# Kernel optimization log

Measured on AMD Instinct MI355X. Metric: run time of the kernel, lower is better.

## Reference

```python
import jax, jax.numpy as jnp
import numpy as np

GRID = 512
F_FEAT = 32
CORE = 16
N_PTS = 2097152
SCALE = 0.1


def _bilinear_sample(plane, coords):
    """plane: (F, H, W); coords: (N, 2) with (x, y) in [-1, 1], align_corners=True.
    Returns (F, N)."""
    F_, H, W = plane.shape
    x = (coords[:, 0] + 1.0) * 0.5 * (W - 1)
    y = (coords[:, 1] + 1.0) * 0.5 * (H - 1)
    x0f = jnp.floor(x)
    y0f = jnp.floor(y)
    wx = x - x0f  # (N,)
    wy = y - y0f
    x0 = jnp.clip(x0f.astype(jnp.int32), 0, W - 1)
    x1 = jnp.clip(x0 + 1, 0, W - 1)
    y0 = jnp.clip(y0f.astype(jnp.int32), 0, H - 1)
    y1 = jnp.clip(y0 + 1, 0, H - 1)
    v00 = plane[:, y0, x0]  # (F, N)
    v01 = plane[:, y0, x1]
    v10 = plane[:, y1, x0]
    v11 = plane[:, y1, x1]
    return (v00 * (1.0 - wx) * (1.0 - wy)
            + v01 * wx * (1.0 - wy)
            + v10 * (1.0 - wx) * wy
            + v11 * wx * wy)


def setup_inputs() -> dict:
    key = jax.random.key(0)
    k1, k2, k3, k4, k5 = jax.random.split(key, 5)
    coords_plane = jax.random.uniform(
        k1, (3, 1, N_PTS, 1, 2), dtype=jnp.float32, minval=-1.0, maxval=1.0)
    plane_xy = SCALE * jax.random.normal(k2, (1, F_FEAT, GRID, GRID), dtype=jnp.float32)
    plane_yz = SCALE * jax.random.normal(k3, (1, F_FEAT, GRID, GRID), dtype=jnp.float32)
    plane_xz = SCALE * jax.random.normal(k4, (1, F_FEAT, GRID, GRID), dtype=jnp.float32)
    core_tensor = jax.random.normal(k5, (CORE, F_FEAT), dtype=jnp.float32)
    return {"coords_plane": coords_plane, "plane_xy": plane_xy,
            "plane_yz": plane_yz, "plane_xz": plane_xz,
            "core_tensor": core_tensor}


def reference(coords_plane, plane_xy, plane_yz, plane_xz, core_tensor):
    # coords_plane: (3, 1, N, 1, 2) -> (3, N, 2)
    c = coords_plane.reshape(3, -1, 2)
    f_xy = _bilinear_sample(plane_xy[0], c[0])  # (F, N)
    f_yz = _bilinear_sample(plane_yz[0], c[1])
    f_xz = _bilinear_sample(plane_xz[0], c[2])
    prod = f_xy * f_yz * f_xz                   # (F, N)
    # sum over core dim: out[f, n] = (sum_k core[k, f]) * prod[f, n]
    scale = jnp.sum(core_tensor, axis=0)        # (F,)
    out = (scale[:, None] * prod).T             # (N, F)
    return out
```

## Files before the change

kernel.cpp:

```cpp
#include <hip/hip_runtime.h>
#include <hip/hip_fp16.h>

#define N_PTS 2097152
#define GRID_ 512
#define F_FEAT 32
#define HW (GRID_ * GRID_)
#define HWF ((size_t)HW * F_FEAT)

#define NBINS 64
#define BIN_SHIFT 3
#define BIN_CAP 40960
#define CUR_STRIDE 32
#define PTS_PER_BLOCK 1024
#define SEGCAP 64
#define BPB 640

typedef float f32x4 __attribute__((ext_vector_type(4)));
typedef unsigned long long u64;

__global__ void td_scale_kernel(const float* __restrict__ core,
                                float* __restrict__ scale) {
    int f = threadIdx.x;
    float s = 0.0f;
#pragma unroll
    for (int k = 0; k < 16; ++k) s += core[k * F_FEAT + f];
    scale[f] = s;
}

__global__ void td_transpose_kernel(const float* __restrict__ pxy,
                                    const float* __restrict__ pyz,
                                    const float* __restrict__ pxz,
                                    const float* __restrict__ scale,
                                    __half* __restrict__ wsh) {
    __shared__ float tile[32][33];
    const int plane = blockIdx.z;
    const float* src = (plane == 0) ? pxy : ((plane == 1) ? pyz : pxz);
    __half* dst = wsh + (size_t)plane * HWF;
    const int y = blockIdx.y;
    const int x0 = blockIdx.x * 32;

    for (int i = threadIdx.y; i < 32; i += 8) {
        tile[i][threadIdx.x] =
            src[(size_t)i * HW + (size_t)y * GRID_ + x0 + threadIdx.x];
    }
    __syncthreads();
    const float sc = (plane == 0) ? scale[threadIdx.x] : 1.0f;
    for (int i = threadIdx.y; i < 32; i += 8) {
        dst[((size_t)(y * GRID_ + x0 + i)) * F_FEAT + threadIdx.x] =
            __float2half(tile[threadIdx.x][i] * sc);
    }
}

__global__ void td_zero_kernel(int* __restrict__ cursor) {
    for (int i = threadIdx.x; i < 3 * NBINS * CUR_STRIDE; i += 256) cursor[i] = 0;
}

__global__ __launch_bounds__(256) void td_bin_kernel(
    const float2* __restrict__ coords, int* __restrict__ cursor,
    u64* __restrict__ recs) {
    __shared__ int lhist[NBINS];
    __shared__ int lbase[NBINS];
    __shared__ u64 lseg[NBINS][SEGCAP];
    const int pl = blockIdx.y;
    const int tid = threadIdx.x;
    const int base_p = blockIdx.x * PTS_PER_BLOCK;
    if (tid < NBINS) lhist[tid] = 0;
    __syncthreads();

    u64 myrec[4];
    int mybin[4], myslot[4];
#pragma unroll
    for (int k = 0; k < 4; ++k) {
        const int p = base_p + k * 256 + tid;
        const float2 c = coords[(size_t)pl * N_PTS + p];
        const float xf = (c.x + 1.0f) * 0.5f * (float)(GRID_ - 1);
        const float yf = (c.y + 1.0f) * 0.5f * (float)(GRID_ - 1);
        const float x0f = floorf(xf);
        const float y0f = floorf(yf);
        const float wx = xf - x0f;
        const float wy = yf - y0f;
        int x0 = min(max((int)x0f, 0), GRID_ - 1);
        int y0 = min(max((int)y0f, 0), GRID_ - 1);
        const int qwx = min(4095, (int)(wx * 4096.0f + 0.5f));
        const int qwy = min(4095, (int)(wy * 4096.0f + 0.5f));
        const int bin = y0 >> BIN_SHIFT;
        myrec[k] = (u64)p | ((u64)x0 << 21) | ((u64)y0 << 30) |
                   ((u64)qwx << 39) | ((u64)qwy << 51);
        mybin[k] = bin;
        myslot[k] = atomicAdd(&lhist[bin], 1);
    }
    __syncthreads();

    if (tid < NBINS) {
        const int cnt = lhist[tid];
        lbase[tid] =
            (cnt > 0) ? atomicAdd(&cursor[(pl * NBINS + tid) * CUR_STRIDE], cnt)
                      : 0;
    }
#pragma unroll
    for (int k = 0; k < 4; ++k)
        if (myslot[k] < SEGCAP) lseg[mybin[k]][myslot[k]] = myrec[k];
    __syncthreads();

#pragma unroll
    for (int k = 0; k < 4; ++k) {
        if (myslot[k] >= SEGCAP) {
            const int gslot = lbase[mybin[k]] + myslot[k];
            if (gslot < BIN_CAP)
                recs[((size_t)pl * NBINS + mybin[k]) * BIN_CAP + gslot] =
                    myrec[k];
        }
    }
    for (int b = 0; b < NBINS; ++b) {
        const int cnt = min(lhist[b], SEGCAP);
        const int gb = lbase[b];
        for (int r = tid; r < cnt; r += 256) {
            if (gb + r < BIN_CAP)
                recs[((size_t)pl * NBINS + b) * BIN_CAP + gb + r] = lseg[b][r];
        }
    }
}

__device__ __forceinline__ void td_sample_core(u64 r, int fq,
                                               const f32x4* __restrict__ tp,
                                               float* s, int* pid_out) {
    const int pid = (int)(r & 0x1FFFFF);
    const int x0 = (int)((r >> 21) & 511);
    const int y0 = (int)((r >> 30) & 511);
    const float wx = (float)((int)((r >> 39) & 4095)) * (1.0f / 4096.0f);
    const float wy = (float)((int)((r >> 51) & 4095)) * (1.0f / 4096.0f);
    const int x1 = min(x0 + 1, GRID_ - 1);
    const int y1 = min(y0 + 1, GRID_ - 1);

    const f32x4 r00 = tp[(size_t)(y0 * GRID_ + x0) * 4 + fq];
    const f32x4 r01 = tp[(size_t)(y0 * GRID_ + x1) * 4 + fq];
    const f32x4 r10 = tp[(size_t)(y1 * GRID_ + x0) * 4 + fq];
    const f32x4 r11 = tp[(size_t)(y1 * GRID_ + x1) * 4 + fq];

    const float w00 = (1.0f - wx) * (1.0f - wy);
    const float w01 = wx * (1.0f - wy);
    const float w10 = (1.0f - wx) * wy;
    const float w11 = wx * wy;

    const half2* h00 = reinterpret_cast<const half2*>(&r00);
    const half2* h01 = reinterpret_cast<const half2*>(&r01);
    const half2* h10 = reinterpret_cast<const half2*>(&r10);
    const half2* h11 = reinterpret_cast<const half2*>(&r11);
#pragma unroll
    for (int j = 0; j < 4; ++j) {
        const float2 f00 = __half22float2(h00[j]);
        const float2 f01 = __half22float2(h01[j]);
        const float2 f10 = __half22float2(h10[j]);
        const float2 f11 = __half22float2(h11[j]);
        s[2 * j] = f00.x * w00 + f01.x * w01 + f10.x * w10 + f11.x * w11;
        s[2 * j + 1] = f00.y * w00 + f01.y * w01 + f10.y * w10 + f11.y * w11;
    }
    *pid_out = pid;
}

__device__ __forceinline__ int td_bin_of_block(int i, int* sub) {
    const int xcd = i & 7;
    const int j = i >> 3;
    const int g = j / BPB;
    *sub = j - g * BPB;
    return g * 8 + xcd;
}

__global__ __launch_bounds__(256) void td_sample_plane_kernel(
    const u64* __restrict__ recs, const int* __restrict__ cursor,
    const f32x4* __restrict__ ws4, f32x4* __restrict__ featline) {
    const int pl = blockIdx.y + 1;
    int sub;
    const int bin = td_bin_of_block(blockIdx.x, &sub);
    const int slot = sub * 64 + (threadIdx.x >> 2);
    const int fq = threadIdx.x & 3;
    const int cnt = min(cursor[(pl * NBINS + bin) * CUR_STRIDE], BIN_CAP);
    if (slot >= cnt) return;

    const u64 r = recs[((size_t)pl * NBINS + bin) * BIN_CAP + slot];
    float s[8];
    int pid;
    td_sample_core(r, fq, ws4 + (size_t)pl * (HWF / 8), s, &pid);

    union {
        f32x4 v;
        half2 h[4];
    } u;
#pragma unroll
    for (int j = 0; j < 4; ++j) u.h[j] = __floats2half2_rn(s[2 * j], s[2 * j + 1]);
    __builtin_nontemporal_store(
        u.v, &featline[(size_t)pid * 8 + (pl - 1) * 4 + fq]);
}

__global__ __launch_bounds__(256) void td_sample_combine_kernel(
    const u64* __restrict__ recs, const int* __restrict__ cursor,
    const f32x4* __restrict__ ws4, const f32x4* __restrict__ featline,
    f32x4* __restrict__ out) {
    int sub;
    const int bin = td_bin_of_block(blockIdx.x, &sub);
    const int slot = sub * 64 + (threadIdx.x >> 2);
    const int fq = threadIdx.x & 3;
    const int cnt = min(cursor[bin * CUR_STRIDE], BIN_CAP);
    if (slot >= cnt) return;

    const u64 r = recs[(size_t)bin * BIN_CAP + slot];
    float s[8];
    int pid;
    td_sample_core(r, fq, ws4, s, &pid);

    union {
        f32x4 v;
        half2 h[4];
    } f1, f2;
    f1.v = featline[(size_t)pid * 8 + fq];
    f2.v = featline[(size_t)pid * 8 + 4 + fq];

    f32x4 o0, o1;
    float rr[8];
#pragma unroll
    for (int j = 0; j < 4; ++j) {
        const float2 a = __half22float2(f1.h[j]);
        const float2 b = __half22float2(f2.h[j]);
        rr[2 * j] = s[2 * j] * a.x * b.x;
        rr[2 * j + 1] = s[2 * j + 1] * a.y * b.y;
    }
    o0.x = rr[0]; o0.y = rr[1]; o0.z = rr[2]; o0.w = rr[3];
    o1.x = rr[4]; o1.y = rr[5]; o1.z = rr[6]; o1.w = rr[7];
    __builtin_nontemporal_store(o0, &out[(size_t)pid * 8 + fq * 2]);
    __builtin_nontemporal_store(o1, &out[(size_t)pid * 8 + fq * 2 + 1]);
}

__global__ __launch_bounds__(256) void td_sample_kernel(
    const float2* __restrict__ coords, const f32x4* __restrict__ ws4,
    f32x4* __restrict__ out) {
    const int tid = blockIdx.x * 256 + threadIdx.x;
    const int p = tid >> 2;
    const int fq = tid & 3;

    const float2 c0 = coords[p];
    const float2 c1 = coords[N_PTS + p];
    const float2 c2 = coords[2 * N_PTS + p];

    size_t idx[3][4];
    float w[3][4];
    const float2 cc[3] = {c0, c1, c2};
#pragma unroll
    for (int pl = 0; pl < 3; ++pl) {
        const float xf = (cc[pl].x + 1.0f) * 0.5f * (float)(GRID_ - 1);
        const float yf = (cc[pl].y + 1.0f) * 0.5f * (float)(GRID_ - 1);
        const float x0f = floorf(xf);
        const float y0f = floorf(yf);
        const float wx = xf - x0f;
        const float wy = yf - y0f;
        int x0 = min(max((int)x0f, 0), GRID_ - 1);
        int y0 = min(max((int)y0f, 0), GRID_ - 1);
        const int x1 = min(x0 + 1, GRID_ - 1);
        const int y1 = min(y0 + 1, GRID_ - 1);
        const size_t base = (size_t)pl * (HWF / 8);
        idx[pl][0] = base + (size_t)(y0 * GRID_ + x0) * 4 + fq;
        idx[pl][1] = base + (size_t)(y0 * GRID_ + x1) * 4 + fq;
        idx[pl][2] = base + (size_t)(y1 * GRID_ + x0) * 4 + fq;
        idx[pl][3] = base + (size_t)(y1 * GRID_ + x1) * 4 + fq;
        w[pl][0] = (1.0f - wx) * (1.0f - wy);
        w[pl][1] = wx * (1.0f - wy);
        w[pl][2] = (1.0f - wx) * wy;
        w[pl][3] = wx * wy;
    }

    f32x4 v[3][4];
#pragma unroll
    for (int pl = 0; pl < 3; ++pl)
#pragma unroll
        for (int cnr = 0; cnr < 4; ++cnr) v[pl][cnr] = ws4[idx[pl][cnr]];

    float prod[8];
#pragma unroll
    for (int j = 0; j < 8; ++j) prod[j] = 1.0f;
#pragma unroll
    for (int pl = 0; pl < 3; ++pl) {
        const half2* h0 = reinterpret_cast<const half2*>(&v[pl][0]);
        const half2* h1 = reinterpret_cast<const half2*>(&v[pl][1]);
        const half2* h2 = reinterpret_cast<const half2*>(&v[pl][2]);
        const half2* h3 = reinterpret_cast<const half2*>(&v[pl][3]);
#pragma unroll
        for (int j = 0; j < 4; ++j) {
            const float2 f00 = __half22float2(h0[j]);
            const float2 f01 = __half22float2(h1[j]);
            const float2 f10 = __half22float2(h2[j]);
            const float2 f11 = __half22float2(h3[j]);
            prod[2 * j] *= f00.x * w[pl][0] + f01.x * w[pl][1] +
                           f10.x * w[pl][2] + f11.x * w[pl][3];
            prod[2 * j + 1] *= f00.y * w[pl][0] + f01.y * w[pl][1] +
                               f10.y * w[pl][2] + f11.y * w[pl][3];
        }
    }

    f32x4 o0, o1;
    o0.x = prod[0]; o0.y = prod[1]; o0.z = prod[2]; o0.w = prod[3];
    o1.x = prod[4]; o1.y = prod[5]; o1.z = prod[6]; o1.w = prod[7];
    __builtin_nontemporal_store(o0, &out[(size_t)tid * 2]);
    __builtin_nontemporal_store(o1, &out[(size_t)tid * 2 + 1]);
}

__global__ __launch_bounds__(256) void td_fallback_kernel(
    const float* __restrict__ coords, const float* __restrict__ pxy,
    const float* __restrict__ pyz, const float* __restrict__ pxz,
    const float* __restrict__ core, float* __restrict__ out) {
    const int tid = blockIdx.x * 256 + threadIdx.x;
    const int p = tid >> 5;
    const int f = tid & 31;

    float s = 0.0f;
#pragma unroll
    for (int k = 0; k < 16; ++k) s += core[k * F_FEAT + f];

    float prod = s;
    const float* planes[3] = {pxy, pyz, pxz};
#pragma unroll
    for (int plane = 0; plane < 3; ++plane) {
        const float cx = coords[((size_t)plane * N_PTS + p) * 2 + 0];
        const float cy = coords[((size_t)plane * N_PTS + p) * 2 + 1];
        const float xf = (cx + 1.0f) * 0.5f * (float)(GRID_ - 1);
        const float yf = (cy + 1.0f) * 0.5f * (float)(GRID_ - 1);
        const float x0f = floorf(xf);
        const float y0f = floorf(yf);
        const float wx = xf - x0f;
        const float wy = yf - y0f;
        int x0 = min(max((int)x0f, 0), GRID_ - 1);
        int y0 = min(max((int)y0f, 0), GRID_ - 1);
        const int x1 = min(x0 + 1, GRID_ - 1);
        const int y1 = min(y0 + 1, GRID_ - 1);
        const float* src = planes[plane] + (size_t)f * HW;
        const float v00 = src[y0 * GRID_ + x0];
        const float v01 = src[y0 * GRID_ + x1];
        const float v10 = src[y1 * GRID_ + x0];
        const float v11 = src[y1 * GRID_ + x1];
        prod *= v00 * (1.0f - wx) * (1.0f - wy) + v01 * wx * (1.0f - wy) +
                v10 * (1.0f - wx) * wy + v11 * wx * wy;
    }
    out[(size_t)p * F_FEAT + f] = prod;
}

extern "C" void kernel_launch(void* const* d_in, const int* in_sizes, int n_in,
                              void* d_out, int out_size, void* d_ws,
                              size_t ws_size, hipStream_t stream) {
    const float* coords = (const float*)d_in[0];
    const float* pxy = (const float*)d_in[1];
    const float* pyz = (const float*)d_in[2];
    const float* pxz = (const float*)d_in[3];
    const float* core = (const float*)d_in[4];
    float* out = (float*)d_out;

    size_t off = 0;
    auto alloc = [&off](size_t bytes) {
        size_t o = off;
        off = (off + bytes + 255) & ~(size_t)255;
        return o;
    };
    const size_t off_wsh = alloc(3 * HWF * sizeof(__half));
    const size_t off_scale = alloc(32 * sizeof(float));
    const size_t need_r4 = off;
    const size_t off_cur = alloc((size_t)3 * NBINS * CUR_STRIDE * sizeof(int));
    const size_t off_recs = alloc((size_t)3 * NBINS * BIN_CAP * sizeof(u64));
    const size_t off_feat = alloc((size_t)N_PTS * 128);
    const size_t need_full = off;

    char* ws = (char*)d_ws;

    if (ws_size >= need_r4) {
        __half* wsh = (__half*)(ws + off_wsh);
        float* scale = (float*)(ws + off_scale);
        td_scale_kernel<<<1, 32, 0, stream>>>(core, scale);
        td_transpose_kernel<<<dim3(GRID_ / 32, GRID_, 3), dim3(32, 8), 0,
                              stream>>>(pxy, pyz, pxz, scale, wsh);
        if (ws_size >= need_full) {
            int* cursor = (int*)(ws + off_cur);
            u64* recs = (u64*)(ws + off_recs);
            f32x4* featline = (f32x4*)(ws + off_feat);
            td_zero_kernel<<<1, 256, 0, stream>>>(cursor);
            td_bin_kernel<<<dim3(N_PTS / PTS_PER_BLOCK, 3), 256, 0, stream>>>(
                (const float2*)coords, cursor, recs);
            td_sample_plane_kernel<<<dim3(NBINS * BPB, 2), 256, 0, stream>>>(
                recs, cursor, (const f32x4*)wsh, featline);
            td_sample_combine_kernel<<<NBINS * BPB, 256, 0, stream>>>(
                recs, cursor, (const f32x4*)wsh, (const f32x4*)featline,
                (f32x4*)out);
        } else {
            td_sample_kernel<<<N_PTS * 4 / 256, 256, 0, stream>>>(
                (const float2*)coords, (const f32x4*)wsh, (f32x4*)out);
        }
    } else {
        td_fallback_kernel<<<N_PTS * 32 / 256, 256, 0, stream>>>(
            coords, pxy, pyz, pxz, core, out);
    }
}
```

Before: 378.5 us.

## Index intermediate plane features by plane-0 sorted slot instead of point id

```diff
diff --git a/kernel.cpp b/kernel.cpp
--- a/kernel.cpp
+++ b/kernel.cpp
@@ -55,13 +55,12 @@
     for (int i = threadIdx.x; i < 3 * NBINS * CUR_STRIDE; i += 256) cursor[i] = 0;
 }
 
-__global__ __launch_bounds__(256) void td_bin_kernel(
+__global__ __launch_bounds__(256) void td_bin0_kernel(
     const float2* __restrict__ coords, int* __restrict__ cursor,
-    u64* __restrict__ recs) {
+    u64* __restrict__ recs0, int* __restrict__ s0map) {
     __shared__ int lhist[NBINS];
     __shared__ int lbase[NBINS];
     __shared__ u64 lseg[NBINS][SEGCAP];
-    const int pl = blockIdx.y;
     const int tid = threadIdx.x;
     const int base_p = blockIdx.x * PTS_PER_BLOCK;
     if (tid < NBINS) lhist[tid] = 0;
@@ -72,7 +71,7 @@
 #pragma unroll
     for (int k = 0; k < 4; ++k) {
         const int p = base_p + k * 256 + tid;
-        const float2 c = coords[(size_t)pl * N_PTS + p];
+        const float2 c = coords[p];
         const float xf = (c.x + 1.0f) * 0.5f * (float)(GRID_ - 1);
         const float yf = (c.y + 1.0f) * 0.5f * (float)(GRID_ - 1);
         const float x0f = floorf(xf);
@@ -94,8 +93,74 @@
     if (tid < NBINS) {
         const int cnt = lhist[tid];
         lbase[tid] =
-            (cnt > 0) ? atomicAdd(&cursor[(pl * NBINS + tid) * CUR_STRIDE], cnt)
-                      : 0;
+            (cnt > 0) ? atomicAdd(&cursor[tid * CUR_STRIDE], cnt) : 0;
+    }
+#pragma unroll
+    for (int k = 0; k < 4; ++k)
+        if (myslot[k] < SEGCAP) lseg[mybin[k]][myslot[k]] = myrec[k];
+    __syncthreads();
+
+#pragma unroll
+    for (int k = 0; k < 4; ++k) {
+        const int p = base_p + k * 256 + tid;
+        int gslot = lbase[mybin[k]] + myslot[k];
+        if (gslot >= BIN_CAP) gslot = BIN_CAP - 1;
+        const int s0 = mybin[k] * BIN_CAP + gslot;
+        s0map[p] = s0;
+        if (myslot[k] >= SEGCAP) recs0[s0] = myrec[k];
+    }
+    for (int b = 0; b < NBINS; ++b) {
+        const int cnt = min(lhist[b], SEGCAP);
+        const int gb = lbase[b];
+        for (int r = tid; r < cnt; r += 256) {
+            if (gb + r < BIN_CAP) recs0[(size_t)b * BIN_CAP + gb + r] = lseg[b][r];
+        }
+    }
+}
+
+__global__ __launch_bounds__(256) void td_bin12_kernel(
+    const float2* __restrict__ coords, const int* __restrict__ s0map,
+    int* __restrict__ cursor, u64* __restrict__ recs12) {
+    __shared__ int lhist[NBINS];
+    __shared__ int lbase[NBINS];
+    __shared__ u64 lseg[NBINS][SEGCAP];
+    const int pl = blockIdx.y + 1;
+    const int tid = threadIdx.x;
+    const int base_p = blockIdx.x * PTS_PER_BLOCK;
+    if (tid < NBINS) lhist[tid] = 0;
+    __syncthreads();
+
+    u64 myrec[4];
+    int mybin[4], myslot[4];
+#pragma unroll
+    for (int k = 0; k < 4; ++k) {
+        const int p = base_p + k * 256 + tid;
+        const float2 c = coords[(size_t)pl * N_PTS + p];
+        const int s0 = s0map[p];
+        const float xf = (c.x + 1.0f) * 0.5f * (float)(GRID_ - 1);
+        const float yf = (c.y + 1.0f) * 0.5f * (float)(GRID_ - 1);
+        const float x0f = floorf(xf);
+        const float y0f = floorf(yf);
+        const float wx = xf - x0f;
+        const float wy = yf - y0f;
+        int x0 = min(max((int)x0f, 0), GRID_ - 1);
+        int y0 = min(max((int)y0f, 0), GRID_ - 1);
+        const int qwx = min(4095, (int)(wx * 4096.0f + 0.5f));
+        const int qwy = min(4095, (int)(wy * 4096.0f + 0.5f));
+        const int bin = y0 >> BIN_SHIFT;
+        myrec[k] = (u64)s0 | ((u64)x0 << 22) | ((u64)y0 << 31) |
+                   ((u64)qwx << 40) | ((u64)qwy << 52);
+        mybin[k] = bin;
+        myslot[k] = atomicAdd(&lhist[bin], 1);
+    }
+    __syncthreads();
+
+    if (tid < NBINS) {
+        const int cnt = lhist[tid];
+        lbase[tid] =
+            (cnt > 0)
+                ? atomicAdd(&cursor[((pl * NBINS) + tid) * CUR_STRIDE], cnt)
+                : 0;
     }
 #pragma unroll
     for (int k = 0; k < 4; ++k)
@@ -107,7 +172,7 @@
         if (myslot[k] >= SEGCAP) {
             const int gslot = lbase[mybin[k]] + myslot[k];
             if (gslot < BIN_CAP)
-                recs[((size_t)pl * NBINS + mybin[k]) * BIN_CAP + gslot] =
+                recs12[(((size_t)(pl - 1) * NBINS + mybin[k]) * BIN_CAP) + gslot] =
                     myrec[k];
         }
     }
@@ -116,19 +181,16 @@
         const int gb = lbase[b];
         for (int r = tid; r < cnt; r += 256) {
             if (gb + r < BIN_CAP)
-                recs[((size_t)pl * NBINS + b) * BIN_CAP + gb + r] = lseg[b][r];
+                recs12[((size_t)(pl - 1) * NBINS + b) * BIN_CAP + gb + r] =
+                    lseg[b][r];
         }
     }
 }
 
-__device__ __forceinline__ void td_sample_core(u64 r, int fq,
+__device__ __forceinline__ void td_sample_core(int x0, int y0, float wx,
+                                               float wy, int fq,
                                                const f32x4* __restrict__ tp,
-                                               float* s, int* pid_out) {
-    const int pid = (int)(r & 0x1FFFFF);
-    const int x0 = (int)((r >> 21) & 511);
-    const int y0 = (int)((r >> 30) & 511);
-    const float wx = (float)((int)((r >> 39) & 4095)) * (1.0f / 4096.0f);
-    const float wy = (float)((int)((r >> 51) & 4095)) * (1.0f / 4096.0f);
+                                               float* s) {
     const int x1 = min(x0 + 1, GRID_ - 1);
     const int y1 = min(y0 + 1, GRID_ - 1);
 
@@ -155,7 +217,6 @@
         s[2 * j] = f00.x * w00 + f01.x * w01 + f10.x * w10 + f11.x * w11;
         s[2 * j + 1] = f00.y * w00 + f01.y * w01 + f10.y * w10 + f11.y * w11;
     }
-    *pid_out = pid;
 }
 
 __device__ __forceinline__ int td_bin_of_block(int i, int* sub) {
@@ -166,9 +227,9 @@
     return g * 8 + xcd;
 }
 
-__global__ __launch_bounds__(256) void td_sample_plane_kernel(
-    const u64* __restrict__ recs, const int* __restrict__ cursor,
-    const f32x4* __restrict__ ws4, f32x4* __restrict__ featline) {
+__global__ __launch_bounds__(256) void td_sample12_kernel(
+    const u64* __restrict__ recs12, const int* __restrict__ cursor,
+    const f32x4* __restrict__ ws4, f32x4* __restrict__ feat) {
     const int pl = blockIdx.y + 1;
     int sub;
     const int bin = td_bin_of_block(blockIdx.x, &sub);
@@ -177,10 +238,15 @@
     const int cnt = min(cursor[(pl * NBINS + bin) * CUR_STRIDE], BIN_CAP);
     if (slot >= cnt) return;
 
-    const u64 r = recs[((size_t)pl * NBINS + bin) * BIN_CAP + slot];
+    const u64 r = recs12[((size_t)(pl - 1) * NBINS + bin) * BIN_CAP + slot];
+    const int s0 = (int)(r & 0x3FFFFF);
+    const int x0 = (int)((r >> 22) & 511);
+    const int y0 = (int)((r >> 31) & 511);
+    const float wx = (float)((int)((r >> 40) & 4095)) * (1.0f / 4096.0f);
+    const float wy = (float)((int)((r >> 52) & 4095)) * (1.0f / 4096.0f);
+
     float s[8];
-    int pid;
-    td_sample_core(r, fq, ws4 + (size_t)pl * (HWF / 8), s, &pid);
+    td_sample_core(x0, y0, wx, wy, fq, ws4 + (size_t)pl * (HWF / 8), s);
 
     union {
         f32x4 v;
@@ -188,13 +254,12 @@
     } u;
 #pragma unroll
     for (int j = 0; j < 4; ++j) u.h[j] = __floats2half2_rn(s[2 * j], s[2 * j + 1]);
-    __builtin_nontemporal_store(
-        u.v, &featline[(size_t)pid * 8 + (pl - 1) * 4 + fq]);
-}
-
-__global__ __launch_bounds__(256) void td_sample_combine_kernel(
-    const u64* __restrict__ recs, const int* __restrict__ cursor,
-    const f32x4* __restrict__ ws4, const f32x4* __restrict__ featline,
+    __builtin_nontemporal_store(u.v, &feat[(size_t)s0 * 8 + (pl - 1) * 4 + fq]);
+}
+
+__global__ __launch_bounds__(256) void td_combine_kernel(
+    const u64* __restrict__ recs0, const int* __restrict__ cursor,
+    const f32x4* __restrict__ ws4, const f32x4* __restrict__ feat,
     f32x4* __restrict__ out) {
     int sub;
     const int bin = td_bin_of_block(blockIdx.x, &sub);
@@ -203,19 +268,24 @@
     const int cnt = min(cursor[bin * CUR_STRIDE], BIN_CAP);
     if (slot >= cnt) return;
 
-    const u64 r = recs[(size_t)bin * BIN_CAP + slot];
+    const size_t s0 = (size_t)bin * BIN_CAP + slot;
+    const u64 r = recs0[s0];
+    const int pid = (int)(r & 0x1FFFFF);
+    const int x0 = (int)((r >> 21) & 511);
+    const int y0 = (int)((r >> 30) & 511);
+    const float wx = (float)((int)((r >> 39) & 4095)) * (1.0f / 4096.0f);
+    const float wy = (float)((int)((r >> 51) & 4095)) * (1.0f / 4096.0f);
+
     float s[8];
-    int pid;
-    td_sample_core(r, fq, ws4, s, &pid);
+    td_sample_core(x0, y0, wx, wy, fq, ws4, s);
 
     union {
         f32x4 v;
         half2 h[4];
     } f1, f2;
-    f1.v = featline[(size_t)pid * 8 + fq];
-    f2.v = featline[(size_t)pid * 8 + 4 + fq];
-
-    f32x4 o0, o1;
+    f1.v = feat[s0 * 8 + fq];
+    f2.v = feat[s0 * 8 + 4 + fq];
+
     float rr[8];
 #pragma unroll
     for (int j = 0; j < 4; ++j) {
@@ -224,6 +294,7 @@
         rr[2 * j] = s[2 * j] * a.x * b.x;
         rr[2 * j + 1] = s[2 * j + 1] * a.y * b.y;
     }
+    f32x4 o0, o1;
     o0.x = rr[0]; o0.y = rr[1]; o0.z = rr[2]; o0.w = rr[3];
     o1.x = rr[4]; o1.y = rr[5]; o1.z = rr[6]; o1.w = rr[7];
     __builtin_nontemporal_store(o0, &out[(size_t)pid * 8 + fq * 2]);
@@ -361,8 +432,10 @@
     const size_t off_scale = alloc(32 * sizeof(float));
     const size_t need_r4 = off;
     const size_t off_cur = alloc((size_t)3 * NBINS * CUR_STRIDE * sizeof(int));
-    const size_t off_recs = alloc((size_t)3 * NBINS * BIN_CAP * sizeof(u64));
-    const size_t off_feat = alloc((size_t)N_PTS * 128);
+    const size_t off_s0map = alloc((size_t)N_PTS * sizeof(int));
+    const size_t off_recs0 = alloc((size_t)NBINS * BIN_CAP * sizeof(u64));
+    const size_t off_recs12 = alloc((size_t)2 * NBINS * BIN_CAP * sizeof(u64));
+    const size_t off_feat = alloc((size_t)NBINS * BIN_CAP * 128);
     const size_t need_full = off;
 
     char* ws = (char*)d_ws;
@@ -375,15 +448,19 @@
                               stream>>>(pxy, pyz, pxz, scale, wsh);
         if (ws_size >= need_full) {
             int* cursor = (int*)(ws + off_cur);
-            u64* recs = (u64*)(ws + off_recs);
-            f32x4* featline = (f32x4*)(ws + off_feat);
+            int* s0map = (int*)(ws + off_s0map);
+            u64* recs0 = (u64*)(ws + off_recs0);
+            u64* recs12 = (u64*)(ws + off_recs12);
+            f32x4* feat = (f32x4*)(ws + off_feat);
             td_zero_kernel<<<1, 256, 0, stream>>>(cursor);
-            td_bin_kernel<<<dim3(N_PTS / PTS_PER_BLOCK, 3), 256, 0, stream>>>(
-                (const float2*)coords, cursor, recs);
-            td_sample_plane_kernel<<<dim3(NBINS * BPB, 2), 256, 0, stream>>>(
-                recs, cursor, (const f32x4*)wsh, featline);
-            td_sample_combine_kernel<<<NBINS * BPB, 256, 0, stream>>>(
-                recs, cursor, (const f32x4*)wsh, (const f32x4*)featline,
+            td_bin0_kernel<<<N_PTS / PTS_PER_BLOCK, 256, 0, stream>>>(
+                (const float2*)coords, cursor, recs0, s0map);
+            td_bin12_kernel<<<dim3(N_PTS / PTS_PER_BLOCK, 2), 256, 0, stream>>>(
+                (const float2*)coords, s0map, cursor, recs12);
+            td_sample12_kernel<<<dim3(NBINS * BPB, 2), 256, 0, stream>>>(
+                recs12, cursor, (const f32x4*)wsh, feat);
+            td_combine_kernel<<<NBINS * BPB, 256, 0, stream>>>(
+                recs0, cursor, (const f32x4*)wsh, (const f32x4*)feat,
                 (f32x4*)out);
         } else {
             td_sample_kernel<<<N_PTS * 4 / 256, 256, 0, stream>>>(
```

Result: slower. 387.5 us (+2.4%).

## Sample all three planes binned, then combine in a coalesced streaming pass

Applied to the files above, without the earlier changes.

```diff
diff --git a/kernel.cpp b/kernel.cpp
--- a/kernel.cpp
+++ b/kernel.cpp
@@ -94,8 +94,9 @@
     if (tid < NBINS) {
         const int cnt = lhist[tid];
         lbase[tid] =
-            (cnt > 0) ? atomicAdd(&cursor[(pl * NBINS + tid) * CUR_STRIDE], cnt)
-                      : 0;
+            (cnt > 0)
+                ? atomicAdd(&cursor[(pl * NBINS + tid) * CUR_STRIDE], cnt)
+                : 0;
     }
 #pragma unroll
     for (int k = 0; k < 4; ++k)
@@ -121,14 +122,10 @@
     }
 }
 
-__device__ __forceinline__ void td_sample_core(u64 r, int fq,
+__device__ __forceinline__ void td_sample_core(int x0, int y0, float wx,
+                                               float wy, int fq,
                                                const f32x4* __restrict__ tp,
-                                               float* s, int* pid_out) {
-    const int pid = (int)(r & 0x1FFFFF);
-    const int x0 = (int)((r >> 21) & 511);
-    const int y0 = (int)((r >> 30) & 511);
-    const float wx = (float)((int)((r >> 39) & 4095)) * (1.0f / 4096.0f);
-    const float wy = (float)((int)((r >> 51) & 4095)) * (1.0f / 4096.0f);
+                                               float* s) {
     const int x1 = min(x0 + 1, GRID_ - 1);
     const int y1 = min(y0 + 1, GRID_ - 1);
 
@@ -155,7 +152,6 @@
         s[2 * j] = f00.x * w00 + f01.x * w01 + f10.x * w10 + f11.x * w11;
         s[2 * j + 1] = f00.y * w00 + f01.y * w01 + f10.y * w10 + f11.y * w11;
     }
-    *pid_out = pid;
 }
 
 __device__ __forceinline__ int td_bin_of_block(int i, int* sub) {
@@ -166,10 +162,10 @@
     return g * 8 + xcd;
 }
 
-__global__ __launch_bounds__(256) void td_sample_plane_kernel(
+__global__ __launch_bounds__(256) void td_sample_binned_kernel(
     const u64* __restrict__ recs, const int* __restrict__ cursor,
-    const f32x4* __restrict__ ws4, f32x4* __restrict__ featline) {
-    const int pl = blockIdx.y + 1;
+    const f32x4* __restrict__ ws4, f32x4* __restrict__ feat) {
+    const int pl = blockIdx.y;
     int sub;
     const int bin = td_bin_of_block(blockIdx.x, &sub);
     const int slot = sub * 64 + (threadIdx.x >> 2);
@@ -178,9 +174,14 @@
     if (slot >= cnt) return;
 
     const u64 r = recs[((size_t)pl * NBINS + bin) * BIN_CAP + slot];
+    const int pid = (int)(r & 0x1FFFFF);
+    const int x0 = (int)((r >> 21) & 511);
+    const int y0 = (int)((r >> 30) & 511);
+    const float wx = (float)((int)((r >> 39) & 4095)) * (1.0f / 4096.0f);
+    const float wy = (float)((int)((r >> 51) & 4095)) * (1.0f / 4096.0f);
+
     float s[8];
-    int pid;
-    td_sample_core(r, fq, ws4 + (size_t)pl * (HWF / 8), s, &pid);
+    td_sample_core(x0, y0, wx, wy, fq, ws4 + (size_t)pl * (HWF / 8), s);
 
     union {
         f32x4 v;
@@ -188,46 +189,38 @@
     } u;
 #pragma unroll
     for (int j = 0; j < 4; ++j) u.h[j] = __floats2half2_rn(s[2 * j], s[2 * j + 1]);
-    __builtin_nontemporal_store(
-        u.v, &featline[(size_t)pid * 8 + (pl - 1) * 4 + fq]);
-}
-
-__global__ __launch_bounds__(256) void td_sample_combine_kernel(
-    const u64* __restrict__ recs, const int* __restrict__ cursor,
-    const f32x4* __restrict__ ws4, const f32x4* __restrict__ featline,
-    f32x4* __restrict__ out) {
-    int sub;
-    const int bin = td_bin_of_block(blockIdx.x, &sub);
-    const int slot = sub * 64 + (threadIdx.x >> 2);
-    const int fq = threadIdx.x & 3;
-    const int cnt = min(cursor[bin * CUR_STRIDE], BIN_CAP);
-    if (slot >= cnt) return;
-
-    const u64 r = recs[(size_t)bin * BIN_CAP + slot];
-    float s[8];
-    int pid;
-    td_sample_core(r, fq, ws4, s, &pid);
-
-    union {
+    __builtin_nontemporal_store(u.v, &feat[(size_t)pid * 12 + pl * 4 + fq]);
+}
+
+__global__ __launch_bounds__(256) void td_combine_stream_kernel(
+    const f32x4* __restrict__ feat, f32x4* __restrict__ out) {
+    const size_t t = (size_t)blockIdx.x * 256 + threadIdx.x;
+    const size_t pid = t >> 2;
+    const int fq = (int)(t & 3);
+
+    union U {
         f32x4 v;
         half2 h[4];
-    } f1, f2;
-    f1.v = featline[(size_t)pid * 8 + fq];
-    f2.v = featline[(size_t)pid * 8 + 4 + fq];
-
+    };
+    U a, b, c;
+    a.v = feat[pid * 12 + fq];
+    b.v = feat[pid * 12 + 4 + fq];
+    c.v = feat[pid * 12 + 8 + fq];
+
+    float rr[8];
+#pragma unroll
+    for (int j = 0; j < 4; ++j) {
+        const float2 fa = __half22float2(a.h[j]);
+        const float2 fb = __half22float2(b.h[j]);
+        const float2 fc = __half22float2(c.h[j]);
+        rr[2 * j] = fa.x * fb.x * fc.x;
+        rr[2 * j + 1] = fa.y * fb.y * fc.y;
+    }
     f32x4 o0, o1;
-    float rr[8];
-#pragma unroll
-    for (int j = 0; j < 4; ++j) {
-        const float2 a = __half22float2(f1.h[j]);
-        const float2 b = __half22float2(f2.h[j]);
-        rr[2 * j] = s[2 * j] * a.x * b.x;
-        rr[2 * j + 1] = s[2 * j + 1] * a.y * b.y;
-    }
     o0.x = rr[0]; o0.y = rr[1]; o0.z = rr[2]; o0.w = rr[3];
     o1.x = rr[4]; o1.y = rr[5]; o1.z = rr[6]; o1.w = rr[7];
-    __builtin_nontemporal_store(o0, &out[(size_t)pid * 8 + fq * 2]);
-    __builtin_nontemporal_store(o1, &out[(size_t)pid * 8 + fq * 2 + 1]);
+    __builtin_nontemporal_store(o0, &out[pid * 8 + fq * 2]);
+    __builtin_nontemporal_store(o1, &out[pid * 8 + fq * 2 + 1]);
 }
 
 __global__ __launch_bounds__(256) void td_sample_kernel(
@@ -362,7 +355,7 @@
     const size_t need_r4 = off;
     const size_t off_cur = alloc((size_t)3 * NBINS * CUR_STRIDE * sizeof(int));
     const size_t off_recs = alloc((size_t)3 * NBINS * BIN_CAP * sizeof(u64));
-    const size_t off_feat = alloc((size_t)N_PTS * 128);
+    const size_t off_feat = alloc((size_t)N_PTS * 192);
     const size_t need_full = off;
 
     char* ws = (char*)d_ws;
@@ -376,15 +369,14 @@
         if (ws_size >= need_full) {
             int* cursor = (int*)(ws + off_cur);
             u64* recs = (u64*)(ws + off_recs);
-            f32x4* featline = (f32x4*)(ws + off_feat);
+            f32x4* feat = (f32x4*)(ws + off_feat);
             td_zero_kernel<<<1, 256, 0, stream>>>(cursor);
             td_bin_kernel<<<dim3(N_PTS / PTS_PER_BLOCK, 3), 256, 0, stream>>>(
                 (const float2*)coords, cursor, recs);
-            td_sample_plane_kernel<<<dim3(NBINS * BPB, 2), 256, 0, stream>>>(
-                recs, cursor, (const f32x4*)wsh, featline);
-            td_sample_combine_kernel<<<NBINS * BPB, 256, 0, stream>>>(
-                recs, cursor, (const f32x4*)wsh, (const f32x4*)featline,
-                (f32x4*)out);
+            td_sample_binned_kernel<<<dim3(NBINS * BPB, 3), 256, 0, stream>>>(
+                recs, cursor, (const f32x4*)wsh, feat);
+            td_combine_stream_kernel<<<N_PTS * 4 / 256, 256, 0, stream>>>(
+                (const f32x4*)feat, (f32x4*)out);
         } else {
             td_sample_kernel<<<N_PTS * 4 / 256, 256, 0, stream>>>(
                 (const float2*)coords, (const f32x4*)wsh, (f32x4*)out);
```

After: 385.0 us. About the same (+1.7%).
